# Performance work log

Hardware: AMD Instinct MI355X
Metric: run time of the kernel (lower is better)

The kernel has to match this reference:

```python
import jax, jax.numpy as jnp
import numpy as np

QMAX = 7.0   # int4 symmetric, narrow range [-7, 7] per weight; acts use [-8, 7]
QMIN = -8.0

def _ste_quant(v, scale, qmin, qmax):
    """Symmetric per-tensor fake-quant with straight-through estimator."""
    s = jax.lax.stop_gradient(scale)
    q = jnp.clip(jnp.round(v / s), qmin, qmax) * s
    return v + jax.lax.stop_gradient(q - v)


def setup_inputs() -> dict:
    key = jax.random.key(0)
    k1, k2, k3 = jax.random.split(key, 3)
    d_model, vocab = 1024, 50257
    x = jax.random.normal(k1, (2, 1024, d_model), jnp.float32)
    W = jax.random.normal(k2, (vocab, d_model), jnp.float32) * 0.02
    b = jax.random.normal(k3, (vocab,), jnp.float32) * 0.01
    return {"x": x, "W": W, "b": b}


def reference(x, W, b):
    # Activation quant: 4-bit signed, per-tensor scale from max-abs stats
    sx = jnp.max(jnp.abs(x)) / QMAX
    xq = _ste_quant(x, sx, QMIN, QMAX)
    # Weight quant: 4-bit signed per-tensor
    sw = jnp.max(jnp.abs(W)) / QMAX
    wq = _ste_quant(W, sw, QMIN, QMAX)
    # Int32 bias: quantized at the accumulator scale sx*sw (range huge -> round only)
    sb = jax.lax.stop_gradient(sx * sw)
    bq = b + jax.lax.stop_gradient(jnp.round(b / sb) * sb - b)
    # Quantized GEMM with int32-style accumulation, expressed as dequantized matmul
    logits = jnp.einsum('bsd,vd->bsv', xq, wq) + bq  # [B, S, vocab]
    return jax.nn.log_softmax(logits, axis=-1)
```

## Files before the change

kernel.cpp:

```cpp
#include <hip/hip_runtime.h>
#include <hip/hip_bf16.h>

#define N_VOCAB 50257
#define NB      400
#define N_PAD   51200
#define D_K     1024
#define M_ROWS  2048

typedef __attribute__((ext_vector_type(4))) int i32x4;

__device__ inline void async_copy16(const void* g, void* l) {
  auto* gp = (const __attribute__((address_space(1))) unsigned int*)g;
  auto* lp = (__attribute__((address_space(3))) unsigned int*)l;
  __builtin_amdgcn_global_load_lds(gp, lp, 16, 0, 0);
}

__device__ inline signed char qint(float v, float s) {
  float q = fminf(fmaxf(rintf(v / s), -8.f), 7.f);
  return (signed char)(int)q;
}

__global__ void absmax_kernel(const float4* __restrict__ p, int n4,
                              unsigned* __restrict__ out) {
  float m = 0.f;
  for (int i = blockIdx.x * blockDim.x + threadIdx.x; i < n4;
       i += gridDim.x * blockDim.x) {
    float4 v = p[i];
    m = fmaxf(m, fmaxf(fmaxf(fabsf(v.x), fabsf(v.y)),
                       fmaxf(fabsf(v.z), fabsf(v.w))));
  }
#pragma unroll
  for (int off = 32; off; off >>= 1) m = fmaxf(m, __shfl_xor(m, off));
  __shared__ float red[4];
  int tid = threadIdx.x;
  if ((tid & 63) == 0) red[tid >> 6] = m;
  __syncthreads();
  if (tid == 0) {
    m = fmaxf(fmaxf(red[0], red[1]), fmaxf(red[2], red[3]));
    atomicMax(out, __float_as_uint(m));
  }
}

__global__ void quant_x_kernel(const float4* __restrict__ x,
                               char4* __restrict__ qx,
                               const unsigned* __restrict__ amax, int n4) {
  int i = blockIdx.x * blockDim.x + threadIdx.x;
  if (i >= n4) return;
  float s = __uint_as_float(amax[0]) * (1.0f / 7.0f);
  float4 v = x[i];
  char4 q;
  q.x = qint(v.x, s); q.y = qint(v.y, s);
  q.z = qint(v.z, s); q.w = qint(v.w, s);
  qx[i] = q;
}

__global__ void quant_w_kernel(const float4* __restrict__ Wp,
                               char4* __restrict__ qw,
                               const unsigned* __restrict__ amax,
                               int n4_valid, int n4_total) {
  int i = blockIdx.x * blockDim.x + threadIdx.x;
  if (i >= n4_total) return;
  char4 q = {0, 0, 0, 0};
  if (i < n4_valid) {
    float s = __uint_as_float(amax[1]) * (1.0f / 7.0f);
    float4 v = Wp[i];
    q.x = qint(v.x, s); q.y = qint(v.y, s);
    q.z = qint(v.z, s); q.w = qint(v.w, s);
  }
  qw[i] = q;
}

__global__ void bq_kernel(const float* __restrict__ b, float* __restrict__ bq,
                          const unsigned* __restrict__ amax) {
  int i = blockIdx.x * blockDim.x + threadIdx.x;
  if (i >= N_PAD) return;
  float v = 0.f;
  if (i < N_VOCAB) {
    float sb = (__uint_as_float(amax[0]) * (1.0f / 7.0f)) *
               (__uint_as_float(amax[1]) * (1.0f / 7.0f));
    v = rintf(b[i] / sb) * sb;
  }
  bq[i] = v;
}

__global__ __launch_bounds__(256, 3) void gemm_kernel(
    const signed char* __restrict__ qx,
    const signed char* __restrict__ qw,
    const float* __restrict__ bq,
    const unsigned* __restrict__ amax,
    float* __restrict__ outp,
    float* __restrict__ pmax,
    float* __restrict__ psum)
{
  constexpr int BK = 64;
  __shared__ signed char sA[2][128 * BK];
  __shared__ signed char sB[2][128 * BK];
  __shared__ float redMax[128][2];
  __shared__ float redSum[128][2];

  const int tid = threadIdx.x;
  const int l = tid & 63;
  const int w = tid >> 6;
  const int wr = w >> 1, wc = w & 1;

  const int bid = blockIdx.x;
  const int vb = (bid & 7) * 800 + (bid >> 3);
  const int nb = vb >> 4;
  const int m0 = (vb & 15) * 128;
  const int n0 = nb * 128;

  const float sx = __uint_as_float(amax[0]) * (1.0f / 7.0f);
  const float sw = __uint_as_float(amax[1]) * (1.0f / 7.0f);
  const float scale = sx * sw;

  i32x4 acc[4][4] = {};

  const int srow = (l >> 2);
  const int sslot = (l & 3) ^ (srow & 3);
  const int scol = sslot * 16;

  auto stage = [&](int buf, int k0) {
#pragma unroll
    for (int i = 0; i < 2; ++i) {
      int c = w * 2 + i;
      int row = c * 16 + srow;
      async_copy16(qx + (size_t)(m0 + row) * D_K + k0 + scol,
                   &sA[buf][c * 1024]);
      async_copy16(qw + (size_t)(n0 + row) * D_K + k0 + scol,
                   &sB[buf][c * 1024]);
    }
  };

  stage(0, 0);
  __syncthreads();

  int cur = 0;
  constexpr int NT = D_K / BK;
  for (int kt = 0; kt < NT; ++kt) {
    if (kt + 1 < NT) stage(cur ^ 1, (kt + 1) * BK);

    i32x4 af[4], bfr[4];
#pragma unroll
    for (int mi = 0; mi < 4; ++mi) {
      int row = wr * 64 + mi * 16 + (l & 15);
      int kb = ((l >> 4) ^ (row & 3)) * 16;
      af[mi] = *(const i32x4*)&sA[cur][row * BK + kb];
    }
#pragma unroll
    for (int ni = 0; ni < 4; ++ni) {
      int row = wc * 64 + ni * 16 + (l & 15);
      int kb = ((l >> 4) ^ (row & 3)) * 16;
      bfr[ni] = *(const i32x4*)&sB[cur][row * BK + kb];
    }
#pragma unroll
    for (int mi = 0; mi < 4; ++mi)
#pragma unroll
      for (int ni = 0; ni < 4; ++ni)
        acc[mi][ni] = __builtin_amdgcn_mfma_i32_16x16x64_i8(
            af[mi], bfr[ni], acc[mi][ni], 0, 0, 0);

    __syncthreads();
    cur ^= 1;
  }

  bool valid[4];
  float bb[4];
#pragma unroll
  for (int ni = 0; ni < 4; ++ni) {
    int col = n0 + wc * 64 + ni * 16 + (l & 15);
    valid[ni] = (col < N_VOCAB);
    bb[ni] = valid[ni] ? bq[col] : 0.f;
  }

  float lg[4][4][4];
#pragma unroll
  for (int mi = 0; mi < 4; ++mi)
#pragma unroll
    for (int ni = 0; ni < 4; ++ni)
#pragma unroll
      for (int r = 0; r < 4; ++r)
        lg[mi][ni][r] = (float)acc[mi][ni][r] * scale + bb[ni];

#pragma unroll
  for (int ni = 0; ni < 4; ++ni) {
    if (valid[ni]) {
      int col = n0 + wc * 64 + ni * 16 + (l & 15);
#pragma unroll
      for (int mi = 0; mi < 4; ++mi)
#pragma unroll
        for (int r = 0; r < 4; ++r) {
          int row = m0 + wr * 64 + mi * 16 + (l >> 4) * 4 + r;
          outp[(size_t)row * N_VOCAB + col] = lg[mi][ni][r];
        }
    }
  }

  float rmax[4][4];
#pragma unroll
  for (int mi = 0; mi < 4; ++mi)
#pragma unroll
    for (int r = 0; r < 4; ++r) {
      float mval = -3.4e38f;
#pragma unroll
      for (int ni = 0; ni < 4; ++ni)
        if (valid[ni]) mval = fmaxf(mval, lg[mi][ni][r]);
#pragma unroll
      for (int off = 1; off < 16; off <<= 1)
        mval = fmaxf(mval, __shfl_xor(mval, off));
      rmax[mi][r] = mval;
      if ((l & 15) == 0)
        redMax[wr * 64 + mi * 16 + (l >> 4) * 4 + r][wc] = mval;
    }
  __syncthreads();

#pragma unroll
  for (int mi = 0; mi < 4; ++mi)
#pragma unroll
    for (int r = 0; r < 4; ++r) {
      int rl = wr * 64 + mi * 16 + (l >> 4) * 4 + r;
      float gmax = fmaxf(redMax[rl][0], redMax[rl][1]);
      float s = 0.f;
#pragma unroll
      for (int ni = 0; ni < 4; ++ni)
        if (valid[ni]) s += __expf(lg[mi][ni][r] - gmax);
#pragma unroll
      for (int off = 1; off < 16; off <<= 1)
        s += __shfl_xor(s, off);
      if ((l & 15) == 0) redSum[rl][wc] = s;
      rmax[mi][r] = gmax;
    }
  __syncthreads();

  if (wc == 0 && (l & 15) == 0) {
#pragma unroll
    for (int mi = 0; mi < 4; ++mi)
#pragma unroll
      for (int r = 0; r < 4; ++r) {
        int rl = wr * 64 + mi * 16 + (l >> 4) * 4 + r;
        int rowg = m0 + rl;
        pmax[(size_t)rowg * NB + nb] = rmax[mi][r];
        psum[(size_t)rowg * NB + nb] = redSum[rl][0] + redSum[rl][1];
      }
  }
}

__global__ __launch_bounds__(256) void finalize_kernel(
    const float* __restrict__ pmax, const float* __restrict__ psum,
    float* __restrict__ logz) {
  const int row = blockIdx.x;
  const float* pm = pmax + (size_t)row * NB;
  const float* ps = psum + (size_t)row * NB;
  const int tid = threadIdx.x;
  __shared__ float red[8];

  float m = -3.4e38f;
  for (int i = tid; i < NB; i += 256) m = fmaxf(m, pm[i]);
#pragma unroll
  for (int off = 32; off; off >>= 1) m = fmaxf(m, __shfl_xor(m, off));
  if ((tid & 63) == 0) red[tid >> 6] = m;
  __syncthreads();
  m = fmaxf(fmaxf(red[0], red[1]), fmaxf(red[2], red[3]));

  float s = 0.f;
  for (int i = tid; i < NB; i += 256) s += ps[i] * __expf(pm[i] - m);
#pragma unroll
  for (int off = 32; off; off >>= 1) s += __shfl_xor(s, off);
  if ((tid & 63) == 0) red[4 + (tid >> 6)] = s;
  __syncthreads();
  if (tid == 0) {
    s = red[4] + red[5] + red[6] + red[7];
    logz[row] = m + __logf(s);
  }
}

__global__ __launch_bounds__(256) void subtract_kernel(
    float4* __restrict__ out, const float* __restrict__ logz, int n4) {
  for (int i = blockIdx.x * blockDim.x + threadIdx.x; i < n4;
       i += gridDim.x * blockDim.x) {
    float4 v = out[i];
    unsigned base = (unsigned)i * 4u;
    v.x -= logz[(base + 0) / N_VOCAB];
    v.y -= logz[(base + 1) / N_VOCAB];
    v.z -= logz[(base + 2) / N_VOCAB];
    v.w -= logz[(base + 3) / N_VOCAB];
    out[i] = v;
  }
}

extern "C" void kernel_launch(void* const* d_in, const int* in_sizes, int n_in,
                              void* d_out, int out_size, void* d_ws,
                              size_t ws_size, hipStream_t stream) {
  const float* x = (const float*)d_in[0];
  const float* W = (const float*)d_in[1];
  const float* b = (const float*)d_in[2];
  float* out = (float*)d_out;

  char* ws = (char*)d_ws;
  unsigned* amax = (unsigned*)ws;
  float* bq = (float*)(ws + 4096);
  float* logz = (float*)(ws + (1ull << 20));
  float* pmax = (float*)(ws + (2ull << 20));
  float* psum = (float*)(ws + (6ull << 20));
  signed char* qx = (signed char*)(ws + (10ull << 20));
  signed char* qw = (signed char*)(ws + (14ull << 20));

  hipMemsetAsync(amax, 0, 8, stream);

  const int nx4 = (M_ROWS * D_K) / 4;
  const int nw4 = (N_VOCAB * D_K) / 4;
  const int nt4 = (N_PAD * D_K) / 4;

  absmax_kernel<<<512, 256, 0, stream>>>((const float4*)x, nx4, amax + 0);
  absmax_kernel<<<2048, 256, 0, stream>>>((const float4*)W, nw4, amax + 1);

  quant_x_kernel<<<nx4 / 256, 256, 0, stream>>>((const float4*)x, (char4*)qx,
                                                amax, nx4);
  quant_w_kernel<<<nt4 / 256, 256, 0, stream>>>((const float4*)W, (char4*)qw,
                                                amax, nw4, nt4);
  bq_kernel<<<(N_PAD + 255) / 256, 256, 0, stream>>>(b, bq, amax);

  gemm_kernel<<<6400, 256, 0, stream>>>(qx, qw, bq, amax, out, pmax, psum);

  finalize_kernel<<<M_ROWS, 256, 0, stream>>>(pmax, psum, logz);

  const int n4 = (M_ROWS * N_VOCAB) / 4;
  subtract_kernel<<<2048, 256, 0, stream>>>((float4*)out, logz, n4);
}
```

Measured before the change: 581.7 us.

## Merge prep kernels, trim vocab padding, stage GEMM stores through LDS

Merges the two absmax launches into one, and the x/W/bias quantization launches into a single kernel. Padding shrinks from 400 to 393 vocab tiles, which cuts wasted GEMM blocks, and occupancy is raised to 4 blocks per CU. The LDS swizzle pattern changes, and the logits epilogue is staged through shared memory so it can issue coalesced float4 global stores instead of scattered scalar stores. The subtract kernel becomes per-row, dropping integer divisions. The costs are extra LDS traffic and more complex edge handling for the unaligned row stride.

```diff
diff --git a/kernel.cpp b/kernel.cpp
--- a/kernel.cpp
+++ b/kernel.cpp
@@ -2,10 +2,12 @@
 #include <hip/hip_bf16.h>
 
 #define N_VOCAB 50257
-#define NB      400
-#define N_PAD   51200
+#define NB      393
+#define N_PAD   50304
 #define D_K     1024
 #define M_ROWS  2048
+#define GEMM_BLOCKS (NB * 16)
+#define PER_XCD     (GEMM_BLOCKS/8)
 
 typedef __attribute__((ext_vector_type(4))) int i32x4;
 
@@ -20,11 +22,16 @@
   return (signed char)(int)q;
 }
 
-__global__ void absmax_kernel(const float4* __restrict__ p, int n4,
-                              unsigned* __restrict__ out) {
+__global__ void absmax2_kernel(const float4* __restrict__ x, int nx4,
+                               const float4* __restrict__ Wp, int nw4,
+                               unsigned* __restrict__ amax) {
+  const bool isx = blockIdx.x < 512;
+  const float4* p = isx ? x : Wp;
+  const int n4 = isx ? nx4 : nw4;
+  const int b0 = isx ? blockIdx.x : blockIdx.x - 512;
+  const int nb = isx ? 512 : (gridDim.x - 512);
   float m = 0.f;
-  for (int i = blockIdx.x * blockDim.x + threadIdx.x; i < n4;
-       i += gridDim.x * blockDim.x) {
+  for (int i = b0 * blockDim.x + threadIdx.x; i < n4; i += nb * blockDim.x) {
     float4 v = p[i];
     m = fmaxf(m, fmaxf(fmaxf(fabsf(v.x), fabsf(v.y)),
                        fmaxf(fabsf(v.z), fabsf(v.w))));
@@ -37,53 +44,52 @@
   __syncthreads();
   if (tid == 0) {
     m = fmaxf(fmaxf(red[0], red[1]), fmaxf(red[2], red[3]));
-    atomicMax(out, __float_as_uint(m));
-  }
-}
-
-__global__ void quant_x_kernel(const float4* __restrict__ x,
-                               char4* __restrict__ qx,
-                               const unsigned* __restrict__ amax, int n4) {
-  int i = blockIdx.x * blockDim.x + threadIdx.x;
-  if (i >= n4) return;
-  float s = __uint_as_float(amax[0]) * (1.0f / 7.0f);
-  float4 v = x[i];
-  char4 q;
-  q.x = qint(v.x, s); q.y = qint(v.y, s);
-  q.z = qint(v.z, s); q.w = qint(v.w, s);
-  qx[i] = q;
-}
-
-__global__ void quant_w_kernel(const float4* __restrict__ Wp,
-                               char4* __restrict__ qw,
-                               const unsigned* __restrict__ amax,
-                               int n4_valid, int n4_total) {
-  int i = blockIdx.x * blockDim.x + threadIdx.x;
-  if (i >= n4_total) return;
-  char4 q = {0, 0, 0, 0};
-  if (i < n4_valid) {
-    float s = __uint_as_float(amax[1]) * (1.0f / 7.0f);
-    float4 v = Wp[i];
+    atomicMax(&amax[isx ? 0 : 1], __float_as_uint(m));
+  }
+}
+
+__global__ void quant_kernel(const float4* __restrict__ x,
+                             const float4* __restrict__ Wp,
+                             const float* __restrict__ b,
+                             char4* __restrict__ qx, char4* __restrict__ qw,
+                             float* __restrict__ bq,
+                             const unsigned* __restrict__ amax) {
+  const int bid = blockIdx.x;
+  const int tid = threadIdx.x;
+  const int nw4 = (N_VOCAB * D_K) / 4;
+  if (bid < 2048) {
+    int i = bid * 256 + tid;
+    float s = __uint_as_float(amax[0]) * (1.0f / 7.0f);
+    float4 v = x[i];
+    char4 q;
     q.x = qint(v.x, s); q.y = qint(v.y, s);
     q.z = qint(v.z, s); q.w = qint(v.w, s);
-  }
-  qw[i] = q;
-}
-
-__global__ void bq_kernel(const float* __restrict__ b, float* __restrict__ bq,
-                          const unsigned* __restrict__ amax) {
-  int i = blockIdx.x * blockDim.x + threadIdx.x;
-  if (i >= N_PAD) return;
-  float v = 0.f;
-  if (i < N_VOCAB) {
-    float sb = (__uint_as_float(amax[0]) * (1.0f / 7.0f)) *
-               (__uint_as_float(amax[1]) * (1.0f / 7.0f));
-    v = rintf(b[i] / sb) * sb;
-  }
-  bq[i] = v;
-}
-
-__global__ __launch_bounds__(256, 3) void gemm_kernel(
+    qx[i] = q;
+  } else if (bid < 2048 + 50304) {
+    int i = (bid - 2048) * 256 + tid;
+    char4 q = {0, 0, 0, 0};
+    if (i < nw4) {
+      float s = __uint_as_float(amax[1]) * (1.0f / 7.0f);
+      float4 v = Wp[i];
+      q.x = qint(v.x, s); q.y = qint(v.y, s);
+      q.z = qint(v.z, s); q.w = qint(v.w, s);
+    }
+    qw[i] = q;
+  } else {
+    int i = (bid - (2048 + 50304)) * 256 + tid;
+    if (i < N_PAD) {
+      float v = 0.f;
+      if (i < N_VOCAB) {
+        float sb = (__uint_as_float(amax[0]) * (1.0f / 7.0f)) *
+                   (__uint_as_float(amax[1]) * (1.0f / 7.0f));
+        v = rintf(b[i] / sb) * sb;
+      }
+      bq[i] = v;
+    }
+  }
+}
+
+__global__ __launch_bounds__(256, 4) void gemm_kernel(
     const signed char* __restrict__ qx,
     const signed char* __restrict__ qw,
     const float* __restrict__ bq,
@@ -93,8 +99,8 @@
     float* __restrict__ psum)
 {
   constexpr int BK = 64;
-  __shared__ signed char sA[2][128 * BK];
-  __shared__ signed char sB[2][128 * BK];
+  __shared__ __align__(16) signed char sA[2][128 * BK];
+  __shared__ __align__(16) signed char sB[2][128 * BK];
   __shared__ float redMax[128][2];
   __shared__ float redSum[128][2];
 
@@ -104,7 +110,7 @@
   const int wr = w >> 1, wc = w & 1;
 
   const int bid = blockIdx.x;
-  const int vb = (bid & 7) * 800 + (bid >> 3);
+  const int vb = (bid & 7) * PER_XCD + (bid >> 3);
   const int nb = vb >> 4;
   const int m0 = (vb & 15) * 128;
   const int n0 = nb * 128;
@@ -116,8 +122,7 @@
   i32x4 acc[4][4] = {};
 
   const int srow = (l >> 2);
-  const int sslot = (l & 3) ^ (srow & 3);
-  const int scol = sslot * 16;
+  const int scol = ((l & 3) ^ ((l >> 3) & 3)) * 16;
 
   auto stage = [&](int buf, int k0) {
 #pragma unroll
@@ -143,13 +148,13 @@
 #pragma unroll
     for (int mi = 0; mi < 4; ++mi) {
       int row = wr * 64 + mi * 16 + (l & 15);
-      int kb = ((l >> 4) ^ (row & 3)) * 16;
+      int kb = ((l >> 4) ^ ((row >> 1) & 3)) * 16;
       af[mi] = *(const i32x4*)&sA[cur][row * BK + kb];
     }
 #pragma unroll
     for (int ni = 0; ni < 4; ++ni) {
       int row = wc * 64 + ni * 16 + (l & 15);
-      int kb = ((l >> 4) ^ (row & 3)) * 16;
+      int kb = ((l >> 4) ^ ((row >> 1) & 3)) * 16;
       bfr[ni] = *(const i32x4*)&sB[cur][row * BK + kb];
     }
 #pragma unroll
@@ -171,7 +176,6 @@
     valid[ni] = (col < N_VOCAB);
     bb[ni] = valid[ni] ? bq[col] : 0.f;
   }
-
   float lg[4][4][4];
 #pragma unroll
   for (int mi = 0; mi < 4; ++mi)
@@ -180,20 +184,6 @@
 #pragma unroll
       for (int r = 0; r < 4; ++r)
         lg[mi][ni][r] = (float)acc[mi][ni][r] * scale + bb[ni];
-
-#pragma unroll
-  for (int ni = 0; ni < 4; ++ni) {
-    if (valid[ni]) {
-      int col = n0 + wc * 64 + ni * 16 + (l & 15);
-#pragma unroll
-      for (int mi = 0; mi < 4; ++mi)
-#pragma unroll
-        for (int r = 0; r < 4; ++r) {
-          int row = m0 + wr * 64 + mi * 16 + (l >> 4) * 4 + r;
-          outp[(size_t)row * N_VOCAB + col] = lg[mi][ni][r];
-        }
-    }
-  }
 
   float rmax[4][4];
 #pragma unroll
@@ -241,6 +231,63 @@
         pmax[(size_t)rowg * NB + nb] = rmax[mi][r];
         psum[(size_t)rowg * NB + nb] = redSum[rl][0] + redSum[rl][1];
       }
+  }
+
+  float* wscr =
+      reinterpret_cast<float*>((w < 2) ? &sA[0][0] : &sB[0][0]) +
+      (w & 1) * 1100;
+  const int q = l >> 4, j = l & 15;
+  const int c0 = (4 - q) & 3;
+
+#pragma unroll
+  for (int mi = 0; mi < 4; ++mi) {
+#pragma unroll
+    for (int ni = 0; ni < 4; ++ni)
+#pragma unroll
+      for (int r = 0; r < 4; ++r)
+        wscr[((l >> 4) * 4 + r) * 65 + ni * 16 + (l & 15)] = lg[mi][ni][r];
+    asm volatile("" ::: "memory");
+#pragma unroll
+    for (int it = 0; it < 4; ++it) {
+      int rl = it * 4 + q;
+      int rowg = m0 + wr * 64 + mi * 16 + rl;
+      size_t rbase = (size_t)rowg * N_VOCAB + n0 + wc * 64;
+      if (j < 15) {
+        int c = c0 + 4 * j;
+        float4 v = *(const float4*)&wscr[rl * 65 + c];
+        int colg = n0 + wc * 64 + c;
+        if (colg + 3 < N_VOCAB) {
+          *(float4*)&outp[rbase + c] = v;
+        } else {
+          const float* vv = (const float*)&v;
+#pragma unroll
+          for (int e = 0; e < 4; ++e)
+            if (colg + e < N_VOCAB) outp[rbase + c + e] = vv[e];
+        }
+      } else if (c0 == 0) {
+        int c = 60;
+        float4 v = *(const float4*)&wscr[rl * 65 + c];
+        int colg = n0 + wc * 64 + c;
+        if (colg + 3 < N_VOCAB) {
+          *(float4*)&outp[rbase + c] = v;
+        } else {
+          const float* vv = (const float*)&v;
+#pragma unroll
+          for (int e = 0; e < 4; ++e)
+            if (colg + e < N_VOCAB) outp[rbase + c + e] = vv[e];
+        }
+      } else {
+        for (int c = 0; c < c0; ++c) {
+          int colg = n0 + wc * 64 + c;
+          if (colg < N_VOCAB) outp[rbase + c] = wscr[rl * 65 + c];
+        }
+        for (int c = c0 + 60; c < 64; ++c) {
+          int colg = n0 + wc * 64 + c;
+          if (colg < N_VOCAB) outp[rbase + c] = wscr[rl * 65 + c];
+        }
+      }
+    }
+    asm volatile("" ::: "memory");
   }
 }
 
@@ -274,17 +321,22 @@
 }
 
 __global__ __launch_bounds__(256) void subtract_kernel(
-    float4* __restrict__ out, const float* __restrict__ logz, int n4) {
-  for (int i = blockIdx.x * blockDim.x + threadIdx.x; i < n4;
-       i += gridDim.x * blockDim.x) {
-    float4 v = out[i];
-    unsigned base = (unsigned)i * 4u;
-    v.x -= logz[(base + 0) / N_VOCAB];
-    v.y -= logz[(base + 1) / N_VOCAB];
-    v.z -= logz[(base + 2) / N_VOCAB];
-    v.w -= logz[(base + 3) / N_VOCAB];
-    out[i] = v;
-  }
+    float* __restrict__ out, const float* __restrict__ logz) {
+  const int row = blockIdx.x;
+  const float lz = logz[row];
+  const size_t base = (size_t)row * N_VOCAB;
+  const int tid = threadIdx.x;
+  const int a = (4 - (row & 3)) & 3;
+  if (tid < a) out[base + tid] -= lz;
+  const int n4 = (N_VOCAB - a) >> 2;
+  float4* p = (float4*)(out + base + a);
+  for (int i = tid; i < n4; i += 256) {
+    float4 v = p[i];
+    v.x -= lz; v.y -= lz; v.z -= lz; v.w -= lz;
+    p[i] = v;
+  }
+  const int done = a + n4 * 4;
+  if (tid < N_VOCAB - done) out[base + done + tid] -= lz;
 }
 
 extern "C" void kernel_launch(void* const* d_in, const int* in_sizes, int n_in,
@@ -308,21 +360,17 @@
 
   const int nx4 = (M_ROWS * D_K) / 4;
   const int nw4 = (N_VOCAB * D_K) / 4;
-  const int nt4 = (N_PAD * D_K) / 4;
-
-  absmax_kernel<<<512, 256, 0, stream>>>((const float4*)x, nx4, amax + 0);
-  absmax_kernel<<<2048, 256, 0, stream>>>((const float4*)W, nw4, amax + 1);
-
-  quant_x_kernel<<<nx4 / 256, 256, 0, stream>>>((const float4*)x, (char4*)qx,
-                                                amax, nx4);
-  quant_w_kernel<<<nt4 / 256, 256, 0, stream>>>((const float4*)W, (char4*)qw,
-                                                amax, nw4, nt4);
-  bq_kernel<<<(N_PAD + 255) / 256, 256, 0, stream>>>(b, bq, amax);
-
-  gemm_kernel<<<6400, 256, 0, stream>>>(qx, qw, bq, amax, out, pmax, psum);
+
+  absmax2_kernel<<<2560, 256, 0, stream>>>((const float4*)x, nx4,
+                                           (const float4*)W, nw4, amax);
+
+  quant_kernel<<<2048 + 50304 + 197, 256, 0, stream>>>(
+      (const float4*)x, (const float4*)W, b, (char4*)qx, (char4*)qw, bq, amax);
+
+  gemm_kernel<<<GEMM_BLOCKS, 256, 0, stream>>>(qx, qw, bq, amax, out, pmax,
+                                               psum);
 
   finalize_kernel<<<M_ROWS, 256, 0, stream>>>(pmax, psum, logz);
 
-  const int n4 = (M_ROWS * N_VOCAB) / 4;
-  subtract_kernel<<<2048, 256, 0, stream>>>((float4*)out, logz, n4);
-}
+  subtract_kernel<<<M_ROWS, 256, 0, stream>>>(out, logz);
+}
```

Result: slower. 608.8 us (+4.6%).
